# Performance work log

Hardware: AMD Instinct MI355X
Metric: run time of the kernel (lower is better)

Reference implementation:

```python
import jax, jax.numpy as jnp
import numpy as np
from jax import lax

EPS = 1e-5

def _zpool(x):
    # cat(max over channel, mean over channel) -> [B,2,H,W]
    return jnp.concatenate([x.max(axis=1, keepdims=True), x.mean(axis=1, keepdims=True)], axis=1)

def _gate(x, w, g, b, m, v):
    # ZPool -> 7x7 conv (2->1, same pad) -> inference BN -> sigmoid -> scale input
    z = _zpool(x)
    y = lax.conv_general_dilated(z, w, (1, 1), [(3, 3), (3, 3)],
                                 dimension_numbers=('NCHW', 'OIHW', 'NCHW'))
    scale = g / jnp.sqrt(v + EPS)
    y = (y - m[None, :, None, None]) * scale[None, :, None, None] + b[None, :, None, None]
    return x * jax.nn.sigmoid(y)


def setup_inputs() -> dict:
    key = jax.random.key(0)
    ks = jax.random.split(key, 8)
    B, C, H, W = 8, 256, 64, 64
    inp = {
        'x': jax.random.normal(ks[0], (B, C, H, W), dtype=jnp.float32),
        'w_cw': jax.random.normal(ks[1], (1, 2, 7, 7), dtype=jnp.float32) * 0.1,
        'g_cw': jnp.ones((1,), jnp.float32), 'b_cw': jnp.zeros((1,), jnp.float32),
        'm_cw': jnp.zeros((1,), jnp.float32), 'v_cw': jnp.ones((1,), jnp.float32),
        'w_hc': jax.random.normal(ks[2], (1, 2, 7, 7), dtype=jnp.float32) * 0.1,
        'g_hc': jnp.ones((1,), jnp.float32), 'b_hc': jnp.zeros((1,), jnp.float32),
        'm_hc': jnp.zeros((1,), jnp.float32), 'v_hc': jnp.ones((1,), jnp.float32),
        'w_hw': jax.random.normal(ks[3], (1, 2, 7, 7), dtype=jnp.float32) * 0.1,
        'g_hw': jnp.ones((1,), jnp.float32), 'b_hw': jnp.zeros((1,), jnp.float32),
        'm_hw': jnp.zeros((1,), jnp.float32), 'v_hw': jnp.ones((1,), jnp.float32),
        'w1d': jax.random.normal(ks[4], (3, 1, 7), dtype=jnp.float32) * 0.1,
    }
    return inp


def reference(x, w_cw, g_cw, b_cw, m_cw, v_cw,
              w_hc, g_hc, b_hc, m_hc, v_hc,
              w_hw, g_hw, b_hw, m_hw, v_hw, w1d):
    # branch 1: attend over (C) with H as channel dim
    b1 = _gate(x.transpose(0, 2, 1, 3), w_cw, g_cw, b_cw, m_cw, v_cw).transpose(0, 2, 1, 3)
    # branch 2: attend with W as channel dim
    b2 = _gate(x.transpose(0, 3, 2, 1), w_hc, g_hc, b_hc, m_hc, v_hc).transpose(0, 3, 2, 1)
    # branch 3: spatial attention in native layout
    b3 = _gate(x, w_hw, g_hw, b_hw, m_hw, v_hw)

    x_out = (b1 + b2 + b3) / 3.0
    pooled = x_out.mean(axis=(2, 3))                     # [B, C]
    logits = lax.conv_general_dilated(pooled[:, None, :], w1d, (1,), [(3, 3)],
                                      dimension_numbers=('NCH', 'OIH', 'NCH'))  # [B,3,C]
    wts = jax.nn.softmax(logits, axis=1)[..., None, None]  # [B,3,C,1,1]
    branches = jnp.stack([b1, b2, b3], axis=1)             # [B,3,C,H,W]
    return (wts * branches).sum(axis=1)
```

## Files before the change

### kernel.cpp

```cpp
#include <hip/hip_runtime.h>
#include <math.h>

#define BB 8
#define CC 256
#define HH 64
#define WW 64
#define EPS 1e-5f
#define PSCALE (1.f / 12288.f)

__global__ __launch_bounds__(256) void pool_kernel(
    const float* __restrict__ x,
    float* __restrict__ z1max, float* __restrict__ z1mean,
    float* __restrict__ z2max, float* __restrict__ z2mean,
    float* __restrict__ z3max, float* __restrict__ z3mean,
    float* __restrict__ pooled)
{
    __shared__ float smem[HH * 65 + 512];
    int blk = blockIdx.x;
    int t = threadIdx.x;

    if (blk < 8) pooled[blk * 256 + t] = 0.f;

    if (blk < BB * CC) {
        int bc = blk;
        int b = bc >> 8, c = bc & 255;
        const float4* xt4 = (const float4*)x + (size_t)bc * 1024;
        float* tile = smem;
        float* red  = smem + HH * 65;

        #pragma unroll
        for (int i = 0; i < 4; ++i) {
            int idx = t + i * 256;
            float4 v = xt4[idx];
            int h = idx >> 4, w0 = (idx & 15) * 4;
            float* d = &tile[h * 65 + w0];
            d[0] = v.x; d[1] = v.y; d[2] = v.z; d[3] = v.w;
        }
        __syncthreads();

        {
            int w = t & 63, hg = t >> 6;
            float m = -INFINITY, s = 0.f;
            #pragma unroll
            for (int i = 0; i < 16; ++i) {
                float v = tile[(hg * 16 + i) * 65 + w];
                m = fmaxf(m, v); s += v;
            }
            red[t] = m; red[256 + t] = s;
        }
        __syncthreads();
        if (t < 64) {
            float m = red[t], s = red[256 + t];
            #pragma unroll
            for (int g = 1; g < 4; ++g) { m = fmaxf(m, red[g * 64 + t]); s += red[256 + g * 64 + t]; }
            z1max [bc * WW + t] = m;
            z1mean[bc * WW + t] = s * (1.f / 64.f);
        }
        __syncthreads();

        {
            int h = t & 63, wg = t >> 6;
            float m = -INFINITY, s = 0.f;
            #pragma unroll
            for (int i = 0; i < 16; ++i) {
                float v = tile[h * 65 + wg * 16 + i];
                m = fmaxf(m, v); s += v;
            }
            red[t] = m; red[256 + t] = s;
        }
        __syncthreads();
        if (t < 64) {
            float m = red[t], s = red[256 + t];
            #pragma unroll
            for (int g = 1; g < 4; ++g) { m = fmaxf(m, red[g * 64 + t]); s += red[256 + g * 64 + t]; }
            z2max [(b * HH + t) * CC + c] = m;
            z2mean[(b * HH + t) * CC + c] = s * (1.f / 64.f);
        }
    } else {
        int bh = blk - BB * CC;
        int b = bh >> 6, h = bh & 63;
        int wq = t & 15, cgp = t >> 4;

        const float4* base = (const float4*)x
            + ((size_t)b * CC * HH * WW + (size_t)h * WW) / 4 + wq;
        float4 m = make_float4(-INFINITY, -INFINITY, -INFINITY, -INFINITY);
        float4 s = make_float4(0.f, 0.f, 0.f, 0.f);
        #pragma unroll 4
        for (int i = 0; i < 16; ++i) {
            float4 v = base[(size_t)(cgp * 16 + i) * 1024];
            m.x = fmaxf(m.x, v.x); m.y = fmaxf(m.y, v.y);
            m.z = fmaxf(m.z, v.z); m.w = fmaxf(m.w, v.w);
            s.x += v.x; s.y += v.y; s.z += v.z; s.w += v.w;
        }
        float4* mred = (float4*)smem;
        float4* sred = (float4*)smem + 256;
        mred[t] = m; sred[t] = s;
        __syncthreads();
        if (t < 16) {
            float4 mm = mred[t], ss = sred[t];
            #pragma unroll
            for (int g = 1; g < 16; ++g) {
                float4 mv = mred[g * 16 + t], sv = sred[g * 16 + t];
                mm.x = fmaxf(mm.x, mv.x); mm.y = fmaxf(mm.y, mv.y);
                mm.z = fmaxf(mm.z, mv.z); mm.w = fmaxf(mm.w, mv.w);
                ss.x += sv.x; ss.y += sv.y; ss.z += sv.z; ss.w += sv.w;
            }
            ss.x *= (1.f / 256.f); ss.y *= (1.f / 256.f);
            ss.z *= (1.f / 256.f); ss.w *= (1.f / 256.f);
            *(float4*)(z3max  + bh * WW + t * 4) = mm;
            *(float4*)(z3mean + bh * WW + t * 4) = ss;
        }
    }
}

__device__ __forceinline__ float conv_gate(
    const float* __restrict__ zm, const float* __restrict__ za,
    const float* __restrict__ wp, const float* gp, const float* bp,
    const float* mp, const float* vp,
    int R, int Cw, int b, int r, int col)
{
    const float* zmb = zm + (size_t)b * R * Cw;
    const float* zab = za + (size_t)b * R * Cw;
    float acc = 0.f;
    #pragma unroll
    for (int dr = 0; dr < 7; ++dr) {
        int rr = r + dr - 3;
        if (rr < 0 || rr >= R) continue;
        #pragma unroll
        for (int dc = 0; dc < 7; ++dc) {
            int cc2 = col + dc - 3;
            if (cc2 < 0 || cc2 >= Cw) continue;
            acc += wp[dr * 7 + dc]      * zmb[rr * Cw + cc2]
                 + wp[49 + dr * 7 + dc] * zab[rr * Cw + cc2];
        }
    }
    float scale = gp[0] * rsqrtf(vp[0] + EPS);
    float y = (acc - mp[0]) * scale + bp[0];
    return 1.f / (1.f + __expf(-y));
}

__global__ __launch_bounds__(256) void gate_kernel(
    const float* __restrict__ x,
    const float* __restrict__ z1max, const float* __restrict__ z1mean,
    const float* __restrict__ w0p, const float* g0, const float* b0,
    const float* m0, const float* v0, float* __restrict__ s1,
    const float* __restrict__ z2max, const float* __restrict__ z2mean,
    const float* __restrict__ w1p, const float* g1, const float* b1,
    const float* m1, const float* v1, float* __restrict__ s2,
    const float* __restrict__ z3max, const float* __restrict__ z3mean,
    const float* __restrict__ w2p, const float* g2, const float* b2,
    const float* m2, const float* v2, float* __restrict__ s3,
    float* __restrict__ pooled)
{
    int blk = blockIdx.x;
    int t = threadIdx.x;

    if (blk < 512) {
        int o = blk * 256 + t;
        int b = o >> 14, rem = o & 16383;
        int r = rem >> 6, col = o & 63;
        float v = conv_gate(z1max, z1mean, w0p, g0, b0, m0, v0, CC, WW, b, r, col);
        s1[o] = v;
        float prod = v * z1mean[o];
        #pragma unroll
        for (int off = 32; off >= 1; off >>= 1) prod += __shfl_down(prod, off);
        if ((t & 63) == 0) atomicAdd(&pooled[o >> 6], 64.f * prod);
    } else if (blk < 1024) {
        int o = (blk - 512) * 256 + t;
        int b = o >> 14, rem = o & 16383;
        int r = rem >> 8, col = o & 255;
        float v = conv_gate(z2max, z2mean, w1p, g1, b1, m1, v1, HH, CC, b, r, col);
        s2[o] = v;
        atomicAdd(&pooled[(b << 8) | col], 64.f * v * z2mean[o]);
    } else {
        __shared__ float s3row[WW];
        int bh = blk - 1024;
        int b = bh >> 6, h = bh & 63;
        if (t < 64) {
            float v = conv_gate(z3max, z3mean, w2p, g2, b2, m2, v2, HH, WW, b, h, t);
            s3[bh * WW + t] = v;
            s3row[t] = v;
        }
        __syncthreads();

        int wv = t >> 6, l = t & 63;
        int c_local = l >> 2, wsub = l & 3;
        const float4* s3q4 = (const float4*)s3row;

        #pragma unroll 1
        for (int pass = 0; pass < 4; ++pass) {
            int c = pass * 64 + (wv << 4) + c_local;
            const float4* xr4 = (const float4*)x
                + ((size_t)(b * 256 + c) * 4096 + h * 64) / 4 + wsub * 4;
            float acc = 0.f;
            #pragma unroll
            for (int j = 0; j < 4; ++j) {
                float4 xv = xr4[j];
                float4 sv = s3q4[wsub * 4 + j];
                acc += xv.x * sv.x + xv.y * sv.y + xv.z * sv.z + xv.w * sv.w;
            }
            acc += __shfl_xor(acc, 1);
            acc += __shfl_xor(acc, 2);
            if (wsub == 0) atomicAdd(&pooled[b * 256 + c], acc);
        }
    }
}

__global__ __launch_bounds__(256) void final_kernel(
    const float* __restrict__ x,
    const float* __restrict__ s1, const float* __restrict__ s2,
    const float* __restrict__ s3, const float* __restrict__ pooled,
    const float* __restrict__ w1d, float* __restrict__ out)
{
    int i4 = blockIdx.x * 256 + threadIdx.x;
    int w0   = (i4 & 15) * 4;
    int rest = i4 >> 4;
    int h = rest & 63; rest >>= 6;
    int c = rest & 255;
    int b = rest >> 8;

    float lg0 = 0.f, lg1 = 0.f, lg2 = 0.f;
    #pragma unroll
    for (int jj = 0; jj < 7; ++jj) {
        int cc2 = c + jj - 3;
        float pv = (cc2 >= 0 && cc2 < CC) ? pooled[b * CC + cc2] : 0.f;
        lg0 += w1d[jj] * pv;
        lg1 += w1d[7 + jj] * pv;
        lg2 += w1d[14 + jj] * pv;
    }
    lg0 *= PSCALE; lg1 *= PSCALE; lg2 *= PSCALE;
    float mx = fmaxf(lg0, fmaxf(lg1, lg2));
    float e0 = __expf(lg0 - mx), e1 = __expf(lg1 - mx), e2 = __expf(lg2 - mx);
    float inv = 1.f / (e0 + e1 + e2);
    float k0 = e0 * inv, k1 = e1 * inv, k2 = e2 * inv;

    const float4 x4  = *(const float4*)(x  + (size_t)i4 * 4);
    const float4 s1v = *(const float4*)(s1 + ((size_t)(b * CC + c)) * WW + w0);
    const float  s2v = s2[(b * HH + h) * CC + c];
    const float4 s3v = *(const float4*)(s3 + ((size_t)(b * HH + h)) * WW + w0);

    float4 o;
    o.x = x4.x * (k0 * s1v.x + k1 * s2v + k2 * s3v.x);
    o.y = x4.y * (k0 * s1v.y + k1 * s2v + k2 * s3v.y);
    o.z = x4.z * (k0 * s1v.z + k1 * s2v + k2 * s3v.z);
    o.w = x4.w * (k0 * s1v.w + k1 * s2v + k2 * s3v.w);
    *(float4*)(out + (size_t)i4 * 4) = o;
}

extern "C" void kernel_launch(void* const* d_in, const int* in_sizes, int n_in,
                              void* d_out, int out_size, void* d_ws, size_t ws_size,
                              hipStream_t stream)
{
    const float* x    = (const float*)d_in[0];
    const float* w_cw = (const float*)d_in[1];
    const float* g_cw = (const float*)d_in[2];
    const float* b_cw = (const float*)d_in[3];
    const float* m_cw = (const float*)d_in[4];
    const float* v_cw = (const float*)d_in[5];
    const float* w_hc = (const float*)d_in[6];
    const float* g_hc = (const float*)d_in[7];
    const float* b_hc = (const float*)d_in[8];
    const float* m_hc = (const float*)d_in[9];
    const float* v_hc = (const float*)d_in[10];
    const float* w_hw = (const float*)d_in[11];
    const float* g_hw = (const float*)d_in[12];
    const float* b_hw = (const float*)d_in[13];
    const float* m_hw = (const float*)d_in[14];
    const float* v_hw = (const float*)d_in[15];
    const float* w1d  = (const float*)d_in[16];
    float* out = (float*)d_out;

    float* ws = (float*)d_ws;
    const size_t N1 = (size_t)BB * CC * WW;
    const size_t N2 = (size_t)BB * HH * CC;
    const size_t N3 = (size_t)BB * HH * WW;
    float* z1max  = ws;
    float* z1mean = z1max  + N1;
    float* z2max  = z1mean + N1;
    float* z2mean = z2max  + N2;
    float* z3max  = z2mean + N2;
    float* z3mean = z3max  + N3;
    float* s1     = z3mean + N3;
    float* s2     = s1 + N1;
    float* s3     = s2 + N2;
    float* pooled = s3 + N3;

    pool_kernel<<<BB * CC + BB * HH, 256, 0, stream>>>(
        x, z1max, z1mean, z2max, z2mean, z3max, z3mean, pooled);

    gate_kernel<<<1536, 256, 0, stream>>>(
        x,
        z1max, z1mean, w_cw, g_cw, b_cw, m_cw, v_cw, s1,
        z2max, z2mean, w_hc, g_hc, b_hc, m_hc, v_hc, s2,
        z3max, z3mean, w_hw, g_hw, b_hw, m_hw, v_hw, s3,
        pooled);

    final_kernel<<<(BB * CC * HH * WW / 4) / 256, 256, 0, stream>>>(
        x, s1, s2, s3, pooled, w1d, out);
}
```

Before: 144.9 us.

## Transpose branch-2 pooled maps to [B,C,H] and hoist softmax weights per block

Branch-2 z-pool outputs are now written contiguously as [B,C,H], which coalesces the pool-kernel stores. The gate kernel runs the 7x7 conv with a transposed weight index so the result is unchanged, and it replaces per-element atomics with a wavefront reduction plus one atomic per row. The final kernel computes the 3-way softmax weights once per block in thread 0 and shares them through LDS, since each block covers a single (b,c), rather than redoing the conv1d and softmax in every thread. The s2 read in the final kernel becomes a near-broadcast load, and the block barrier is a small added cost.

```diff
diff --git a/kernel.cpp b/kernel.cpp
--- a/kernel.cpp
+++ b/kernel.cpp
@@ -11,7 +11,7 @@
 __global__ __launch_bounds__(256) void pool_kernel(
     const float* __restrict__ x,
     float* __restrict__ z1max, float* __restrict__ z1mean,
-    float* __restrict__ z2max, float* __restrict__ z2mean,
+    float* __restrict__ z2tmax, float* __restrict__ z2tmean,
     float* __restrict__ z3max, float* __restrict__ z3mean,
     float* __restrict__ pooled)
 {
@@ -23,7 +23,6 @@
 
     if (blk < BB * CC) {
         int bc = blk;
-        int b = bc >> 8, c = bc & 255;
         const float4* xt4 = (const float4*)x + (size_t)bc * 1024;
         float* tile = smem;
         float* red  = smem + HH * 65;
@@ -73,8 +72,8 @@
             float m = red[t], s = red[256 + t];
             #pragma unroll
             for (int g = 1; g < 4; ++g) { m = fmaxf(m, red[g * 64 + t]); s += red[256 + g * 64 + t]; }
-            z2max [(b * HH + t) * CC + c] = m;
-            z2mean[(b * HH + t) * CC + c] = s * (1.f / 64.f);
+            z2tmax [bc * HH + t] = m;
+            z2tmean[bc * HH + t] = s * (1.f / 64.f);
         }
     } else {
         int bh = blk - BB * CC;
@@ -113,6 +112,7 @@
     }
 }
 
+template<int TR>
 __device__ __forceinline__ float conv_gate(
     const float* __restrict__ zm, const float* __restrict__ za,
     const float* __restrict__ wp, const float* gp, const float* bp,
@@ -130,8 +130,9 @@
         for (int dc = 0; dc < 7; ++dc) {
             int cc2 = col + dc - 3;
             if (cc2 < 0 || cc2 >= Cw) continue;
-            acc += wp[dr * 7 + dc]      * zmb[rr * Cw + cc2]
-                 + wp[49 + dr * 7 + dc] * zab[rr * Cw + cc2];
+            const int wi = TR ? (dc * 7 + dr) : (dr * 7 + dc);
+            acc += wp[wi]      * zmb[rr * Cw + cc2]
+                 + wp[49 + wi] * zab[rr * Cw + cc2];
         }
     }
     float scale = gp[0] * rsqrtf(vp[0] + EPS);
@@ -144,7 +145,7 @@
     const float* __restrict__ z1max, const float* __restrict__ z1mean,
     const float* __restrict__ w0p, const float* g0, const float* b0,
     const float* m0, const float* v0, float* __restrict__ s1,
-    const float* __restrict__ z2max, const float* __restrict__ z2mean,
+    const float* __restrict__ z2tmax, const float* __restrict__ z2tmean,
     const float* __restrict__ w1p, const float* g1, const float* b1,
     const float* m1, const float* v1, float* __restrict__ s2,
     const float* __restrict__ z3max, const float* __restrict__ z3mean,
@@ -159,7 +160,7 @@
         int o = blk * 256 + t;
         int b = o >> 14, rem = o & 16383;
         int r = rem >> 6, col = o & 63;
-        float v = conv_gate(z1max, z1mean, w0p, g0, b0, m0, v0, CC, WW, b, r, col);
+        float v = conv_gate<0>(z1max, z1mean, w0p, g0, b0, m0, v0, CC, WW, b, r, col);
         s1[o] = v;
         float prod = v * z1mean[o];
         #pragma unroll
@@ -168,16 +169,19 @@
     } else if (blk < 1024) {
         int o = (blk - 512) * 256 + t;
         int b = o >> 14, rem = o & 16383;
-        int r = rem >> 8, col = o & 255;
-        float v = conv_gate(z2max, z2mean, w1p, g1, b1, m1, v1, HH, CC, b, r, col);
+        int r = rem >> 6, col = o & 63;
+        float v = conv_gate<1>(z2tmax, z2tmean, w1p, g1, b1, m1, v1, CC, HH, b, r, col);
         s2[o] = v;
-        atomicAdd(&pooled[(b << 8) | col], 64.f * v * z2mean[o]);
+        float prod = v * z2tmean[o];
+        #pragma unroll
+        for (int off = 32; off >= 1; off >>= 1) prod += __shfl_down(prod, off);
+        if ((t & 63) == 0) atomicAdd(&pooled[o >> 6], 64.f * prod);
     } else {
         __shared__ float s3row[WW];
         int bh = blk - 1024;
         int b = bh >> 6, h = bh & 63;
         if (t < 64) {
-            float v = conv_gate(z3max, z3mean, w2p, g2, b2, m2, v2, HH, WW, b, h, t);
+            float v = conv_gate<0>(z3max, z3mean, w2p, g2, b2, m2, v2, HH, WW, b, h, t);
             s3[bh * WW + t] = v;
             s3row[t] = v;
         }
@@ -212,31 +216,37 @@
     const float* __restrict__ s3, const float* __restrict__ pooled,
     const float* __restrict__ w1d, float* __restrict__ out)
 {
-    int i4 = blockIdx.x * 256 + threadIdx.x;
-    int w0   = (i4 & 15) * 4;
+    __shared__ float kk[3];
+    int t = threadIdx.x;
+    int i4 = blockIdx.x * 256 + t;
     int rest = i4 >> 4;
-    int h = rest & 63; rest >>= 6;
-    int c = rest & 255;
-    int b = rest >> 8;
-
-    float lg0 = 0.f, lg1 = 0.f, lg2 = 0.f;
-    #pragma unroll
-    for (int jj = 0; jj < 7; ++jj) {
-        int cc2 = c + jj - 3;
-        float pv = (cc2 >= 0 && cc2 < CC) ? pooled[b * CC + cc2] : 0.f;
-        lg0 += w1d[jj] * pv;
-        lg1 += w1d[7 + jj] * pv;
-        lg2 += w1d[14 + jj] * pv;
+    int h = rest & 63;
+    int c = (rest >> 6) & 255;
+    int b = rest >> 14;
+
+    if (t == 0) {
+        float lg0 = 0.f, lg1 = 0.f, lg2 = 0.f;
+        #pragma unroll
+        for (int jj = 0; jj < 7; ++jj) {
+            int cc2 = c + jj - 3;
+            float pv = (cc2 >= 0 && cc2 < CC) ? pooled[b * CC + cc2] : 0.f;
+            lg0 += w1d[jj] * pv;
+            lg1 += w1d[7 + jj] * pv;
+            lg2 += w1d[14 + jj] * pv;
+        }
+        lg0 *= PSCALE; lg1 *= PSCALE; lg2 *= PSCALE;
+        float mx = fmaxf(lg0, fmaxf(lg1, lg2));
+        float e0 = __expf(lg0 - mx), e1 = __expf(lg1 - mx), e2 = __expf(lg2 - mx);
+        float inv = 1.f / (e0 + e1 + e2);
+        kk[0] = e0 * inv; kk[1] = e1 * inv; kk[2] = e2 * inv;
     }
-    lg0 *= PSCALE; lg1 *= PSCALE; lg2 *= PSCALE;
-    float mx = fmaxf(lg0, fmaxf(lg1, lg2));
-    float e0 = __expf(lg0 - mx), e1 = __expf(lg1 - mx), e2 = __expf(lg2 - mx);
-    float inv = 1.f / (e0 + e1 + e2);
-    float k0 = e0 * inv, k1 = e1 * inv, k2 = e2 * inv;
-
+    __syncthreads();
+    float k0 = kk[0], k1 = kk[1], k2 = kk[2];
+
+    int w0 = (i4 & 15) * 4;
     const float4 x4  = *(const float4*)(x  + (size_t)i4 * 4);
     const float4 s1v = *(const float4*)(s1 + ((size_t)(b * CC + c)) * WW + w0);
-    const float  s2v = s2[(b * HH + h) * CC + c];
+    const float  s2v = s2[rest];
     const float4 s3v = *(const float4*)(s3 + ((size_t)(b * HH + h)) * WW + w0);
 
     float4 o;
@@ -272,26 +282,26 @@
 
     float* ws = (float*)d_ws;
     const size_t N1 = (size_t)BB * CC * WW;
-    const size_t N2 = (size_t)BB * HH * CC;
+    const size_t N2 = (size_t)BB * CC * HH;
     const size_t N3 = (size_t)BB * HH * WW;
-    float* z1max  = ws;
-    float* z1mean = z1max  + N1;
-    float* z2max  = z1mean + N1;
-    float* z2mean = z2max  + N2;
-    float* z3max  = z2mean + N2;
-    float* z3mean = z3max  + N3;
-    float* s1     = z3mean + N3;
-    float* s2     = s1 + N1;
-    float* s3     = s2 + N2;
-    float* pooled = s3 + N3;
+    float* z1max   = ws;
+    float* z1mean  = z1max   + N1;
+    float* z2tmax  = z1mean  + N1;
+    float* z2tmean = z2tmax  + N2;
+    float* z3max   = z2tmean + N2;
+    float* z3mean  = z3max   + N3;
+    float* s1      = z3mean  + N3;
+    float* s2      = s1 + N1;
+    float* s3      = s2 + N2;
+    float* pooled  = s3 + N3;
 
     pool_kernel<<<BB * CC + BB * HH, 256, 0, stream>>>(
-        x, z1max, z1mean, z2max, z2mean, z3max, z3mean, pooled);
+        x, z1max, z1mean, z2tmax, z2tmean, z3max, z3mean, pooled);
 
     gate_kernel<<<1536, 256, 0, stream>>>(
         x,
         z1max, z1mean, w_cw, g_cw, b_cw, m_cw, v_cw, s1,
-        z2max, z2mean, w_hc, g_hc, b_hc, m_hc, v_hc, s2,
+        z2tmax, z2tmean, w_hc, g_hc, b_hc, m_hc, v_hc, s2,
         z3max, z3mean, w_hw, g_hw, b_hw, m_hw, v_hw, s3,
         pooled);
 
```

Result: faster. 141.7 us (-2.2%).
